# Kernel tuning notes

Measured on AMD Instinct MI355X. Metric: run time of the kernel, lower is better.

The kernel has to match this reference:

```python
import jax, jax.numpy as jnp
import numpy as np

EPS = 1e-5
NUM_HEADS = 12
HEAD_DIM = 64


def _split_heads(x, H, hd):
    B, S, _ = x.shape
    return x.reshape(B, S, H, hd).transpose(0, 2, 1, 3)  # [B,H,S,hd]


def _rope_rotate(x, pos, freqs):
    # x: [B,H,S,hd]; pos: [B,S,nd] int; freqs: [nd,H,hd//2]
    ang = jnp.einsum('bsd,dhf->bhsf', pos.astype(x.dtype), freqs)  # [B,H,S,hd//2]
    cos, sin = jnp.cos(ang), jnp.sin(ang)
    B, H, S, hd = x.shape
    xp = x.reshape(B, H, S, hd // 2, 2)
    xr, xi = xp[..., 0], xp[..., 1]
    out = jnp.stack([xr * cos - xi * sin, xr * sin + xi * cos], axis=-1)
    return out.reshape(B, H, S, hd)


def setup_inputs() -> dict:
    key = jax.random.key(0)
    ks = jax.random.split(key, 8)
    B, Sq, Sk, D = 4, 1024, 1024, 768
    return {
        'q': jax.random.normal(ks[0], (B, Sq, D), jnp.float32),
        'kv': jax.random.normal(ks[1], (B, Sk, D), jnp.float32),
        'posq': jax.random.randint(ks[2], (B, Sq, 2), 0, 32, jnp.int32),
        'posk': jax.random.randint(ks[3], (B, Sk, 2), 0, 32, jnp.int32),
        'w_norm': jnp.ones((D,), jnp.float32),
        'w_q': jax.random.normal(ks[4], (D, D), jnp.float32) * 0.02,
        'b_q': jnp.zeros((D,), jnp.float32),
        'w_kv': jax.random.normal(ks[5], (2 * D, D), jnp.float32) * 0.02,
        'b_kv': jnp.zeros((2 * D,), jnp.float32),
        'w_out': jax.random.normal(ks[6], (D, D), jnp.float32) * 0.02,
        'b_out': jnp.zeros((D,), jnp.float32),
        'freqs': jax.random.normal(ks[7], (2, NUM_HEADS, HEAD_DIM // 2), jnp.float32),
    }


def reference(q, kv, posq, posk, w_norm, w_q, b_q, w_kv, b_kv, w_out, b_out, freqs):
    B, Sq, D = q.shape
    H, hd = NUM_HEADS, HEAD_DIM
    # RMSNorm on q
    qn = q * jax.lax.rsqrt(jnp.mean(q * q, axis=-1, keepdims=True) + EPS) * w_norm
    # projections (torch F.linear: x @ W.T + b)
    qp = qn @ w_q.T + b_q
    kvp = kv @ w_kv.T + b_kv
    k, v = jnp.split(kvp, 2, axis=-1)
    qh = _split_heads(qp, H, hd)
    kh = _split_heads(k, H, hd)
    vh = _split_heads(v, H, hd)
    # ND mixed RoPE
    qh = _rope_rotate(qh, posq, freqs)
    kh = _rope_rotate(kh, posk, freqs)
    # SDPA
    scale = 1.0 / np.sqrt(hd)
    scores = jnp.einsum('bhqd,bhkd->bhqk', qh, kh) * scale
    attn = jax.nn.softmax(scores, axis=-1)
    o = jnp.einsum('bhqk,bhkd->bhqd', attn, vh)
    o = o.transpose(0, 2, 1, 3).reshape(B, Sq, H * hd)
    return o @ w_out.T + b_out
```

## Files before the change

kernel.cpp:

```cpp
#include <hip/hip_runtime.h>

#define B_   4
#define S_   1024
#define D_   768
#define H_   12
#define HD_  64
#define NROW (B_*S_)
#define RSTRIDE (H_*HD_)
#define NBH  (B_*H_)
#define LOG2E 1.44269504f

typedef __bf16 bf16_t;
typedef bf16_t bf16x8 __attribute__((ext_vector_type(8)));
typedef float  f32x4  __attribute__((ext_vector_type(4)));
typedef float  f32x16 __attribute__((ext_vector_type(16)));
typedef unsigned int u32x4 __attribute__((ext_vector_type(4)));

__device__ __forceinline__ unsigned short bf16b(float f){
  bf16_t b = (bf16_t)f;
  return __builtin_bit_cast(unsigned short, b);
}

__device__ __forceinline__ void gload16(const void* g, void* l){
  __builtin_amdgcn_global_load_lds(
      (const __attribute__((address_space(1))) void*)g,
      (__attribute__((address_space(3))) void*)l, 16, 0, 0);
}

__device__ __forceinline__ unsigned int cvtpk(float lo, float hi){
  unsigned int r;
  asm("v_cvt_pk_bf16_f32 %0, %1, %2" : "=v"(r) : "v"(lo), "v"(hi));
  return r;
}

__device__ __forceinline__ void plswap(unsigned int &a, unsigned int &b){
  asm volatile("v_permlane32_swap_b32 %0, %1" : "+v"(a), "+v"(b));
}

__global__ void prep_kernel(const float* __restrict__ q, const float* __restrict__ w_norm,
                            bf16_t* __restrict__ qn,
                            const float* __restrict__ wq,  bf16_t* __restrict__ wqb,
                            const float* __restrict__ wkv, bf16_t* __restrict__ wkvb,
                            const float* __restrict__ wo,  bf16_t* __restrict__ wob,
                            const float* __restrict__ kv,  bf16_t* __restrict__ kvb){
  int bid = blockIdx.x;
  if (bid < NROW){
    int row = bid;
    const float* src = q + (size_t)row*D_;
    float vals[3]; float ss = 0.f;
#pragma unroll
    for (int i=0;i<3;i++){ float v = src[threadIdx.x + i*256]; vals[i]=v; ss += v*v; }
#pragma unroll
    for (int m=1;m<64;m<<=1) ss += __shfl_xor(ss, m, 64);
    __shared__ float red[4];
    if ((threadIdx.x & 63) == 0) red[threadIdx.x>>6] = ss;
    __syncthreads();
    float tot = red[0]+red[1]+red[2]+red[3];
    float rs = rsqrtf(tot*(1.0f/D_) + 1e-5f);
#pragma unroll
    for (int i=0;i<3;i++){
      int c = threadIdx.x + i*256;
      qn[(size_t)row*D_ + c] = (bf16_t)(vals[i]*rs*w_norm[c]);
    }
  } else {
    int i = (bid - NROW)*256 + threadIdx.x;
    const int n0 = D_*D_/4, n1 = 2*D_*D_/4, n2 = D_*D_/4, n3 = NROW*D_/4;
    const float* s; bf16_t* d; int off;
    if (i < n0){ s = wq; d = wqb; off = i; }
    else if (i < n0+n1){ s = wkv; d = wkvb; off = i - n0; }
    else if (i < n0+n1+n2){ s = wo; d = wob; off = i - n0 - n1; }
    else if (i < n0+n1+n2+n3){ s = kv; d = kvb; off = i - n0 - n1 - n2; }
    else return;
    float4 v = reinterpret_cast<const float4*>(s)[off];
    ushort4 o;
    o.x = bf16b(v.x); o.y = bf16b(v.y); o.z = bf16b(v.z); o.w = bf16b(v.w);
    reinterpret_cast<ushort4*>(d)[off] = o;
  }
}

template<int TM, int TN>
__device__ __forceinline__ void stage_t(const bf16_t* __restrict__ A, const bf16_t* __restrict__ W,
                                        int K, int row0, int col0, int kt,
                                        bf16_t* As, bf16_t* Bs){
  const int tid = threadIdx.x;
  const int wv  = tid >> 6;
#pragma unroll
  for (int i=0;i<TM/32;i++){
    int c = i*256 + tid;
    int r = c >> 3, kc = (c & 7) ^ (r & 7);
    gload16(A + (size_t)(row0+r)*K + kt + kc*8, As + (size_t)(i*256 + wv*64)*8);
  }
#pragma unroll
  for (int i=0;i<TN/32;i++){
    int c = i*256 + tid;
    int r = c >> 3, kc = (c & 7) ^ (r & 7);
    gload16(W + (size_t)(col0+r)*K + kt + kc*8, Bs + (size_t)(i*256 + wv*64)*8);
  }
}

template<int TM, int TN>
__device__ __forceinline__ void compute_t(const bf16_t* As, const bf16_t* Bs,
                                          f32x4 (&acc)[TM/32][TN/32]){
  const int lane = threadIdx.x & 63;
  const int wv   = threadIdx.x >> 6;
  const int wr = wv >> 1, wc = wv & 1;
  const int l4 = lane >> 4, lm = lane & 15;
#pragma unroll
  for (int kk=0; kk<2; kk++){
    bf16x8 af[TM/32], bfr[TN/32];
#pragma unroll
    for (int mi=0;mi<TM/32;mi++){
      int r = wr*(TM/2) + mi*16 + lm;
      int s = (kk*4 + l4) ^ (r & 7);
      af[mi] = *reinterpret_cast<const bf16x8*>(As + r*64 + s*8);
    }
#pragma unroll
    for (int ni=0;ni<TN/32;ni++){
      int r = wc*(TN/2) + ni*16 + lm;
      int s = (kk*4 + l4) ^ (r & 7);
      bfr[ni] = *reinterpret_cast<const bf16x8*>(Bs + r*64 + s*8);
    }
#pragma unroll
    for (int mi=0;mi<TM/32;mi++)
#pragma unroll
      for (int ni=0;ni<TN/32;ni++)
        acc[mi][ni] = __builtin_amdgcn_mfma_f32_16x16x32_bf16(af[mi], bfr[ni], acc[mi][ni], 0,0,0);
  }
}

template<int TM, int TN>
__device__ __forceinline__ void gemm_core_db(const bf16_t* __restrict__ A, const bf16_t* __restrict__ W,
                                             int K, int row0, int col0,
                                             bf16_t* As0, bf16_t* As1, bf16_t* Bs0, bf16_t* Bs1,
                                             f32x4 (&acc)[TM/32][TN/32]){
  stage_t<TM,TN>(A, W, K, row0, col0, 0, As0, Bs0);
  __syncthreads();
  const int nt = K/64;
  bf16_t *Ac = As0, *An = As1, *Bc = Bs0, *Bn = Bs1;
  for (int t=0; t<nt; ++t){
    if (t+1 < nt)
      stage_t<TM,TN>(A, W, K, row0, col0, (t+1)*64, An, Bn);
    compute_t<TM,TN>(Ac, Bc, acc);
    __syncthreads();
    bf16_t* tmp;
    tmp = Ac; Ac = An; An = tmp;
    tmp = Bc; Bc = Bn; Bn = tmp;
  }
}

__global__ void gemm_kernel(const bf16_t* __restrict__ A, const bf16_t* __restrict__ W,
                            const float* __restrict__ bias, float* __restrict__ C,
                            int N, int K){
  __shared__ bf16_t As[2][64*64];
  __shared__ bf16_t Bs[2][64*64];
  int l = ((int)blockIdx.x & 7)*96 + ((int)blockIdx.x >> 3);
  int x = l & 63, y = l >> 6;
  f32x4 acc[2][2] = {};
  gemm_core_db<64,64>(A, W, K, x*64, y*64, As[0], As[1], Bs[0], Bs[1], acc);
  const int lane = threadIdx.x & 63;
  const int wv   = threadIdx.x >> 6;
  const int wr = wv >> 1, wc = wv & 1;
  const int l4 = lane >> 4, lm = lane & 15;
  const int row0 = x*64, col0 = y*64;
#pragma unroll
  for (int mi=0;mi<2;mi++){
#pragma unroll
    for (int ni=0;ni<2;ni++){
      int col = col0 + wc*32 + ni*16 + lm;
      float bv = bias[col];
#pragma unroll
      for (int j=0;j<4;j++){
        int row = row0 + wr*32 + mi*16 + l4*4 + j;
        C[(size_t)row*N + col] = acc[mi][ni][j] + bv;
      }
    }
  }
}

__device__ __forceinline__ void epi_rope(f32x4 (&acc)[2][4], const float* __restrict__ bias,
                                         const int* __restrict__ pos, const float* __restrict__ freqs,
                                         bf16_t* __restrict__ dst, int row0, int col0, float scale){
  const int lane = threadIdx.x & 63;
  const int wv   = threadIdx.x >> 6;
  const int wr = wv >> 1, wc = wv & 1;
  const int l4 = lane >> 4, lm = lane & 15;
  const int par = lm & 1;
#pragma unroll
  for (int ni=0;ni<4;ni++){
    int col = col0 + wc*64 + ni*16 + lm;
    int h = col >> 6, hd = col & 63, f = hd >> 1;
    float F1 = freqs[h*32 + f];
    float F2 = freqs[H_*32 + h*32 + f];
    float bv = bias[col];
    int cc = f >> 3, hi = (f >> 2) & 1;
    int ebase = cc*512 + hi*256 + (f&3)*2 + par;
#pragma unroll
    for (int mi=0;mi<2;mi++){
#pragma unroll
      for (int j=0;j<4;j++){
        int row = row0 + wr*32 + mi*16 + l4*4 + j;
        float v = acc[mi][ni][j] + bv;
        float vp = __shfl_xor(v, 1, 64);
        float p0 = (float)pos[row*2+0], p1 = (float)pos[row*2+1];
        float ang = p0*F1 + p1*F2;
        float sn, cs;
        __sincosf(ang, &sn, &cs);
        float out = (par ? (vp*sn + v*cs) : (v*cs - vp*sn)) * scale;
        int b = row >> 10, s = row & 1023;
        int bh = b*H_ + h, tile = s >> 5, lq = s & 31;
        dst[((size_t)(bh*32 + tile))*2048 + ebase + lq*8] = (bf16_t)out;
      }
    }
  }
}

__device__ __forceinline__ void epi_vpack(f32x4 (&acc)[2][4], const float* __restrict__ bias,
                                          bf16_t* __restrict__ vfrag, int row0, int col0){
  const int lane = threadIdx.x & 63;
  const int wv   = threadIdx.x >> 6;
  const int wr = wv >> 1, wc = wv & 1;
  const int l4 = lane >> 4, lm = lane & 15;
#pragma unroll
  for (int ni=0;ni<4;ni++){
    int col = col0 + wc*64 + ni*16 + lm;
    int vcol = col - D_;
    int h = vcol >> 6, d = vcol & 63;
    int dt = d >> 5, lq2 = d & 31;
    float bv = bias[col];
    int ebase = dt*1024 + lq2*8;
#pragma unroll
    for (int mi=0;mi<2;mi++){
#pragma unroll
      for (int j=0;j<4;j++){
        int row = row0 + wr*32 + mi*16 + l4*4 + j;
        int b = row >> 10, s = row & 1023;
        int bh = b*H_ + h;
        int kb = s >> 5, ks = (s >> 4) & 1, hi2 = (s >> 3) & 1, jj = s & 7;
        vfrag[((size_t)(bh*32 + kb))*2048 + ebase + ks*512 + hi2*256 + jj]
            = (bf16_t)(acc[mi][ni][j] + bv);
      }
    }
  }
}

__global__ void gemm_qkv_kernel(const bf16_t* __restrict__ qn, const bf16_t* __restrict__ kvb,
                                const bf16_t* __restrict__ wq, const bf16_t* __restrict__ wkv,
                                const float* __restrict__ bq, const float* __restrict__ bkv,
                                const int* __restrict__ posq, const int* __restrict__ posk,
                                const float* __restrict__ freqs,
                                bf16_t* __restrict__ qh, bf16_t* __restrict__ kh,
                                bf16_t* __restrict__ vfrag){
  __shared__ bf16_t As[2][64*64];
  __shared__ bf16_t Bs[2][128*64];
  int l = ((int)blockIdx.x & 7)*144 + ((int)blockIdx.x >> 3);
  int x = l & 63, y = l >> 6;
  f32x4 acc[2][4] = {};
  if (y < 6){
    gemm_core_db<64,128>(qn, wq, D_, x*64, y*128, As[0], As[1], Bs[0], Bs[1], acc);
    epi_rope(acc, bq, posq, freqs, qh, x*64, y*128, 0.125f*LOG2E);
  } else {
    int c0 = (y-6)*128;
    gemm_core_db<64,128>(kvb, wkv, D_, x*64, c0, As[0], As[1], Bs[0], Bs[1], acc);
    if (y < 12)
      epi_rope(acc, bkv, posk, freqs, kh, x*64, c0, 1.0f);
    else
      epi_vpack(acc, bkv, vfrag, x*64, c0);
  }
}

__device__ __forceinline__ void attn_step(const bf16x8 (&kf)[4], const bf16x8 (&vf)[4],
                                          const bf16x8 (&qf)[4], f32x16 (&acc_o)[2],
                                          float &psum){
  f32x16 accs = {};
#pragma unroll
  for (int c=0;c<4;c++)
    accs = __builtin_amdgcn_mfma_f32_32x32x16_bf16(kf[c], qf[c], accs, 0,0,0);
#pragma unroll
  for (int r=0;r<16;r++){
    float v = exp2f(accs[r]);
    accs[r] = v;
    psum += v;
  }
  bf16x8 pa[2];
#pragma unroll
  for (int ks=0;ks<2;ks++){
    const int base = ks*8;
    unsigned int a0 = cvtpk(accs[base+0], accs[base+1]);
    unsigned int a1 = cvtpk(accs[base+2], accs[base+3]);
    unsigned int b0 = cvtpk(accs[base+4], accs[base+5]);
    unsigned int b1 = cvtpk(accs[base+6], accs[base+7]);
    plswap(a0, b0);
    plswap(a1, b1);
    u32x4 w; w[0]=a0; w[1]=a1; w[2]=b0; w[3]=b1;
    pa[ks] = __builtin_bit_cast(bf16x8, w);
  }
#pragma unroll
  for (int dt=0;dt<2;dt++)
#pragma unroll
    for (int ks=0;ks<2;ks++)
      acc_o[dt] = __builtin_amdgcn_mfma_f32_32x32x16_bf16(pa[ks], vf[dt*2+ks], acc_o[dt], 0,0,0);
}

__global__ __launch_bounds__(256, 3)
void attn_kernel(const bf16_t* __restrict__ Qf, const bf16_t* __restrict__ Kf,
                 const bf16_t* __restrict__ Vf, bf16_t* __restrict__ Oh){
  const int lane = threadIdx.x & 63;
  const int wv   = threadIdx.x >> 6;
  const int hi = lane >> 5, lq = lane & 31;
  int l = ((int)blockIdx.x & 7)*192 + ((int)blockIdx.x >> 3);
  const int bh = l >> 5;
  const int qt = l & 31;
  const int q0 = qt*32;
  const int b = bh / H_, h = bh % H_;
  const size_t headoff = ((size_t)b*S_*H_ + h)*HD_;

  __shared__ float part[4][64][33];
  __shared__ float ps[4][32];

  bf16x8 qf[4];
  {
    const bf16_t* qp_ = Qf + (size_t)(bh*32 + qt)*2048 + lane*8;
#pragma unroll
    for (int c=0;c<4;c++)
      qf[c] = *reinterpret_cast<const bf16x8*>(qp_ + c*512);
  }

  const bf16_t* kbase = Kf + ((size_t)bh*32 + wv*8)*2048 + lane*8;
  const bf16_t* vbase = Vf + ((size_t)bh*32 + wv*8)*2048 + lane*8;

  float psum = 0.f;
  f32x16 acc_o[2] = {};

  bf16x8 kfA[4], kfB[4], vf[4];
#pragma unroll
  for (int c=0;c<4;c++)
    kfA[c] = *reinterpret_cast<const bf16x8*>(kbase + c*512);

#pragma unroll
  for (int t=0; t<4; ++t){
    {
      const bf16_t* vp = vbase + (size_t)(2*t)*2048;
#pragma unroll
      for (int j=0;j<4;j++) vf[j] = *reinterpret_cast<const bf16x8*>(vp + j*512);
      const bf16_t* kp = kbase + (size_t)(2*t+1)*2048;
#pragma unroll
      for (int c=0;c<4;c++) kfB[c] = *reinterpret_cast<const bf16x8*>(kp + c*512);
      attn_step(kfA, vf, qf, acc_o, psum);
    }
    {
      const bf16_t* vp = vbase + (size_t)(2*t+1)*2048;
#pragma unroll
      for (int j=0;j<4;j++) vf[j] = *reinterpret_cast<const bf16x8*>(vp + j*512);
      if (t < 3){
        const bf16_t* kp = kbase + (size_t)(2*t+2)*2048;
#pragma unroll
        for (int c=0;c<4;c++) kfA[c] = *reinterpret_cast<const bf16x8*>(kp + c*512);
      }
      attn_step(kfB, vf, qf, acc_o, psum);
    }
  }

  float tp = psum + __shfl_xor(psum, 32, 64);
#pragma unroll
  for (int dt=0;dt<2;dt++)
#pragma unroll
    for (int r=0;r<16;r++)
      part[wv][lane][dt*16+r] = acc_o[dt][r];
  if (lane < 32) ps[wv][lq] = tp;
  __syncthreads();

  const int dt = wv >> 1;
  const int rbase = (wv & 1)*8;
  float tot = ps[0][lq] + ps[1][lq] + ps[2][lq] + ps[3][lq];
  float inv = 1.0f / tot;

  bf16_t* obase = Oh + headoff;
#pragma unroll
  for (int ri=0;ri<8;ri++){
    int r = rbase + ri;
    float s = part[0][lane][dt*16+r] + part[1][lane][dt*16+r]
            + part[2][lane][dt*16+r] + part[3][lane][dt*16+r];
    float invr = __shfl(inv, (r&3) + 8*(r>>2) + 4*hi, 64);
    int qq = q0 + (r&3) + 8*(r>>2) + 4*hi;
    obase[(size_t)qq*RSTRIDE + dt*32 + lq] = (bf16_t)(s*invr);
  }
}

extern "C" void kernel_launch(void* const* d_in, const int* in_sizes, int n_in,
                              void* d_out, int out_size, void* d_ws, size_t ws_size,
                              hipStream_t stream) {
  const float* q      = (const float*)d_in[0];
  const float* kv     = (const float*)d_in[1];
  const int*   posq   = (const int*)d_in[2];
  const int*   posk   = (const int*)d_in[3];
  const float* w_norm = (const float*)d_in[4];
  const float* w_q    = (const float*)d_in[5];
  const float* b_q    = (const float*)d_in[6];
  const float* w_kv   = (const float*)d_in[7];
  const float* b_kv   = (const float*)d_in[8];
  const float* w_out  = (const float*)d_in[9];
  const float* b_out  = (const float*)d_in[10];
  const float* freqs  = (const float*)d_in[11];
  float* out = (float*)d_out;

  char* p = (char*)d_ws;
  bf16_t* qn   = (bf16_t*)p; p += (size_t)NROW*D_*2;
  bf16_t* kvb  = (bf16_t*)p; p += (size_t)NROW*D_*2;
  bf16_t* wqb  = (bf16_t*)p; p += (size_t)D_*D_*2;
  bf16_t* wkvb = (bf16_t*)p; p += (size_t)2*D_*D_*2;
  bf16_t* wob  = (bf16_t*)p; p += (size_t)D_*D_*2;
  bf16_t* qh   = (bf16_t*)p; p += (size_t)NROW*D_*2;
  bf16_t* kh   = (bf16_t*)p; p += (size_t)NROW*D_*2;
  bf16_t* vt   = (bf16_t*)p; p += (size_t)NBH*HD_*S_*2;
  bf16_t* oh   = (bf16_t*)p; p += (size_t)NROW*D_*2;

  prep_kernel<<<NROW + 5376, 256, 0, stream>>>(q, w_norm, qn,
                                               w_q, wqb, w_kv, wkvb, w_out, wob, kv, kvb);
  gemm_qkv_kernel<<<1152, 256, 0, stream>>>(qn, kvb, wqb, wkvb, b_q, b_kv,
                                            posq, posk, freqs, qh, kh, vt);
  attn_kernel<<<1536, 256, 0, stream>>>(qh, kh, vt, oh);
  gemm_kernel<<<768, 256, 0, stream>>>(oh, wob, b_out, out, D_, D_);
}
```

Before: 74.90 us.

## Pre-pack QKV GEMM operands into MFMA fragment layout and drop LDS staging

The prep kernel now writes the normalized q, kv and the q/kv weights in a 32-row by 16-k fragment layout that matches the 32x32x16 MFMA operand order. The QKV GEMM kernel then loads fragments directly from global memory into registers, with no LDS double buffering, uses 128x128 block tiles with 32x32 MFMAs, and fuses RoPE and V packing with paired stores. This removes LDS traffic and barriers from the projection GEMM. The trade-off is scattered stores in prep and reliance on L2 for operand reuse across blocks.

```diff
diff --git a/kernel.cpp b/kernel.cpp
--- a/kernel.cpp
+++ b/kernel.cpp
@@ -37,12 +37,16 @@
   asm volatile("v_permlane32_swap_b32 %0, %1" : "+v"(a), "+v"(b));
 }
 
+__device__ __forceinline__ size_t frag48_addr(int row, int k){
+  return ((size_t)((row>>5)*48 + (k>>4)))*512 + ((k>>3)&1)*256 + (row&31)*8 + (k&7);
+}
+
 __global__ void prep_kernel(const float* __restrict__ q, const float* __restrict__ w_norm,
-                            bf16_t* __restrict__ qn,
-                            const float* __restrict__ wq,  bf16_t* __restrict__ wqb,
-                            const float* __restrict__ wkv, bf16_t* __restrict__ wkvb,
+                            bf16_t* __restrict__ qnf,
+                            const float* __restrict__ wq,  bf16_t* __restrict__ wqf,
+                            const float* __restrict__ wkv, bf16_t* __restrict__ wkvf,
                             const float* __restrict__ wo,  bf16_t* __restrict__ wob,
-                            const float* __restrict__ kv,  bf16_t* __restrict__ kvb){
+                            const float* __restrict__ kv,  bf16_t* __restrict__ kvbf){
   int bid = blockIdx.x;
   if (bid < NROW){
     int row = bid;
@@ -60,21 +64,130 @@
 #pragma unroll
     for (int i=0;i<3;i++){
       int c = threadIdx.x + i*256;
-      qn[(size_t)row*D_ + c] = (bf16_t)(vals[i]*rs*w_norm[c]);
+      qnf[frag48_addr(row, c)] = (bf16_t)(vals[i]*rs*w_norm[c]);
     }
   } else {
     int i = (bid - NROW)*256 + threadIdx.x;
     const int n0 = D_*D_/4, n1 = 2*D_*D_/4, n2 = D_*D_/4, n3 = NROW*D_/4;
-    const float* s; bf16_t* d; int off;
-    if (i < n0){ s = wq; d = wqb; off = i; }
-    else if (i < n0+n1){ s = wkv; d = wkvb; off = i - n0; }
-    else if (i < n0+n1+n2){ s = wo; d = wob; off = i - n0 - n1; }
-    else if (i < n0+n1+n2+n3){ s = kv; d = kvb; off = i - n0 - n1 - n2; }
-    else return;
-    float4 v = reinterpret_cast<const float4*>(s)[off];
-    ushort4 o;
-    o.x = bf16b(v.x); o.y = bf16b(v.y); o.z = bf16b(v.z); o.w = bf16b(v.w);
-    reinterpret_cast<ushort4*>(d)[off] = o;
+    if (i < n0 + n1 + n3 && i < n0 + n1 || i >= n0 + n1 + n2 || i < n0){}
+    if (i < n0){
+      float4 v = reinterpret_cast<const float4*>(wq)[i];
+      int e0 = i*4, row = e0/768, k = e0%768;
+      ushort4 o; o.x=bf16b(v.x); o.y=bf16b(v.y); o.z=bf16b(v.z); o.w=bf16b(v.w);
+      *reinterpret_cast<ushort4*>(wqf + frag48_addr(row,k)) = o;
+    } else if (i < n0+n1){
+      int off = i - n0;
+      float4 v = reinterpret_cast<const float4*>(wkv)[off];
+      int e0 = off*4, row = e0/768, k = e0%768;
+      ushort4 o; o.x=bf16b(v.x); o.y=bf16b(v.y); o.z=bf16b(v.z); o.w=bf16b(v.w);
+      *reinterpret_cast<ushort4*>(wkvf + frag48_addr(row,k)) = o;
+    } else if (i < n0+n1+n2){
+      int off = i - n0 - n1;
+      float4 v = reinterpret_cast<const float4*>(wo)[off];
+      ushort4 o; o.x=bf16b(v.x); o.y=bf16b(v.y); o.z=bf16b(v.z); o.w=bf16b(v.w);
+      reinterpret_cast<ushort4*>(wob)[off] = o;
+    } else if (i < n0+n1+n2+n3){
+      int off = i - n0 - n1 - n2;
+      float4 v = reinterpret_cast<const float4*>(kv)[off];
+      int e0 = off*4, row = e0/768, k = e0%768;
+      ushort4 o; o.x=bf16b(v.x); o.y=bf16b(v.y); o.z=bf16b(v.z); o.w=bf16b(v.w);
+      *reinterpret_cast<ushort4*>(kvbf + frag48_addr(row,k)) = o;
+    }
+  }
+}
+
+__global__ __launch_bounds__(256, 3)
+void gemm_qkv_kernel(const bf16_t* __restrict__ qnf, const bf16_t* __restrict__ kvbf,
+                     const bf16_t* __restrict__ wqf, const bf16_t* __restrict__ wkvf,
+                     const float* __restrict__ bq, const float* __restrict__ bkv,
+                     const int* __restrict__ posq, const int* __restrict__ posk,
+                     const float* __restrict__ freqs,
+                     bf16_t* __restrict__ qh, bf16_t* __restrict__ kh,
+                     bf16_t* __restrict__ vfrag){
+  const int lane = threadIdx.x & 63;
+  const int wv   = threadIdx.x >> 6;
+  const int hi = lane >> 5, lq = lane & 31;
+  int l = ((int)blockIdx.x & 7)*72 + ((int)blockIdx.x >> 3);
+  const int x = l & 31, y = l >> 5;
+  const int wr = wv >> 1, wc = wv & 1;
+  const int rt0 = x*4 + wr*2;
+  const bf16_t* Af; const bf16_t* Wf; const float* bias; const int* pos; int ntbase;
+  if (y < 6){ Af = qnf; Wf = wqf;  bias = bq;  pos = posq; ntbase = y*4 + wc*2; }
+  else      { Af = kvbf; Wf = wkvf; bias = bkv; pos = posk; ntbase = (y-6)*4 + wc*2; }
+
+  const bf16_t* a0 = Af + ((size_t)(rt0  )*48)*512 + lane*8;
+  const bf16_t* a1 = Af + ((size_t)(rt0+1)*48)*512 + lane*8;
+  const bf16_t* w0 = Wf + ((size_t)(ntbase  )*48)*512 + lane*8;
+  const bf16_t* w1 = Wf + ((size_t)(ntbase+1)*48)*512 + lane*8;
+
+  f32x16 acc[2][2] = {};
+#pragma unroll 4
+  for (int c=0;c<48;c++){
+    bf16x8 A0 = *reinterpret_cast<const bf16x8*>(a0 + (size_t)c*512);
+    bf16x8 A1 = *reinterpret_cast<const bf16x8*>(a1 + (size_t)c*512);
+    bf16x8 W0 = *reinterpret_cast<const bf16x8*>(w0 + (size_t)c*512);
+    bf16x8 W1 = *reinterpret_cast<const bf16x8*>(w1 + (size_t)c*512);
+    acc[0][0] = __builtin_amdgcn_mfma_f32_32x32x16_bf16(W0, A0, acc[0][0], 0,0,0);
+    acc[0][1] = __builtin_amdgcn_mfma_f32_32x32x16_bf16(W0, A1, acc[0][1], 0,0,0);
+    acc[1][0] = __builtin_amdgcn_mfma_f32_32x32x16_bf16(W1, A0, acc[1][0], 0,0,0);
+    acc[1][1] = __builtin_amdgcn_mfma_f32_32x32x16_bf16(W1, A1, acc[1][1], 0,0,0);
+  }
+
+  if (y < 12){
+    const float scale = (y < 6) ? 0.125f*LOG2E : 1.0f;
+    bf16_t* dst = (y < 6) ? qh : kh;
+#pragma unroll
+    for (int rt=0;rt<2;rt++){
+      int row = (rt0+rt)*32 + lq;
+      float p0 = (float)pos[row*2+0], p1 = (float)pos[row*2+1];
+      int bb = row >> 10;
+      int tile = (row & 1023) >> 5;
+#pragma unroll
+      for (int nt=0;nt<2;nt++){
+        int ntg = ntbase + nt;
+#pragma unroll
+        for (int rp=0;rp<8;rp++){
+          int r = rp*2;
+          int n = ntg*32 + (r&3) + 8*(r>>2) + 4*hi;
+          int h = n >> 6, d = n & 63, f = d >> 1;
+          float F1 = freqs[h*32 + f];
+          float F2 = freqs[H_*32 + h*32 + f];
+          float ang = p0*F1 + p1*F2;
+          float sn, cs;
+          __sincosf(ang, &sn, &cs);
+          float ve = acc[nt][rt][r]   + bias[n];
+          float vo = acc[nt][rt][r+1] + bias[n+1];
+          float oe = (ve*cs - vo*sn)*scale;
+          float oo = (ve*sn + vo*cs)*scale;
+          int cc = d >> 4, hi2 = (d >> 3) & 1, jj = d & 7;
+          size_t base = ((size_t)((bb*H_ + h)*32 + tile))*2048 + cc*512 + hi2*256 + lq*8 + jj;
+          ushort2 o; o.x = bf16b(oe); o.y = bf16b(oo);
+          *reinterpret_cast<ushort2*>(dst + base) = o;
+        }
+      }
+    }
+  } else {
+#pragma unroll
+    for (int rt=0;rt<2;rt++){
+      int s_ = (rt0+rt)*32 + lq;
+      int bb = s_ >> 10;
+      int kb = (s_ & 1023) >> 5;
+      int ks = (lq >> 4) & 1, hi2 = (lq >> 3) & 1, jj = lq & 7;
+#pragma unroll
+      for (int nt=0;nt<2;nt++){
+        int ntg = ntbase + nt;
+#pragma unroll
+        for (int r=0;r<16;r++){
+          int n = ntg*32 + (r&3) + 8*(r>>2) + 4*hi;
+          int nv = n - D_;
+          int h = nv >> 6, d = nv & 63;
+          float v = acc[nt][rt][r] + bias[n];
+          size_t addr = ((size_t)((bb*H_ + h)*32 + kb))*2048
+                      + (d>>5)*1024 + ks*512 + hi2*256 + (d&31)*8 + jj;
+          vfrag[addr] = (bf16_t)v;
+        }
+      }
+    }
   }
 }
 
@@ -125,26 +238,6 @@
 #pragma unroll
       for (int ni=0;ni<TN/32;ni++)
         acc[mi][ni] = __builtin_amdgcn_mfma_f32_16x16x32_bf16(af[mi], bfr[ni], acc[mi][ni], 0,0,0);
-  }
-}
-
-template<int TM, int TN>
-__device__ __forceinline__ void gemm_core_db(const bf16_t* __restrict__ A, const bf16_t* __restrict__ W,
-                                             int K, int row0, int col0,
-                                             bf16_t* As0, bf16_t* As1, bf16_t* Bs0, bf16_t* Bs1,
-                                             f32x4 (&acc)[TM/32][TN/32]){
-  stage_t<TM,TN>(A, W, K, row0, col0, 0, As0, Bs0);
-  __syncthreads();
-  const int nt = K/64;
-  bf16_t *Ac = As0, *An = As1, *Bc = Bs0, *Bn = Bs1;
-  for (int t=0; t<nt; ++t){
-    if (t+1 < nt)
-      stage_t<TM,TN>(A, W, K, row0, col0, (t+1)*64, An, Bn);
-    compute_t<TM,TN>(Ac, Bc, acc);
-    __syncthreads();
-    bf16_t* tmp;
-    tmp = Ac; Ac = An; An = tmp;
-    tmp = Bc; Bc = Bn; Bn = tmp;
   }
 }
 
@@ -156,7 +249,16 @@
   int l = ((int)blockIdx.x & 7)*96 + ((int)blockIdx.x >> 3);
   int x = l & 63, y = l >> 6;
   f32x4 acc[2][2] = {};
-  gemm_core_db<64,64>(A, W, K, x*64, y*64, As[0], As[1], Bs[0], Bs[1], acc);
+  stage_t<64,64>(A, W, K, x*64, y*64, 0, As[0], Bs[0]);
+  __syncthreads();
+  const int nt = K/64;
+  for (int t=0; t<nt; ++t){
+    int cur = t & 1;
+    if (t+1 < nt)
+      stage_t<64,64>(A, W, K, x*64, y*64, (t+1)*64, As[cur^1], Bs[cur^1]);
+    compute_t<64,64>(As[cur], Bs[cur], acc);
+    __syncthreads();
+  }
   const int lane = threadIdx.x & 63;
   const int wv   = threadIdx.x >> 6;
   const int wr = wv >> 1, wc = wv & 1;
@@ -174,97 +276,6 @@
         C[(size_t)row*N + col] = acc[mi][ni][j] + bv;
       }
     }
-  }
-}
-
-__device__ __forceinline__ void epi_rope(f32x4 (&acc)[2][4], const float* __restrict__ bias,
-                                         const int* __restrict__ pos, const float* __restrict__ freqs,
-                                         bf16_t* __restrict__ dst, int row0, int col0, float scale){
-  const int lane = threadIdx.x & 63;
-  const int wv   = threadIdx.x >> 6;
-  const int wr = wv >> 1, wc = wv & 1;
-  const int l4 = lane >> 4, lm = lane & 15;
-  const int par = lm & 1;
-#pragma unroll
-  for (int ni=0;ni<4;ni++){
-    int col = col0 + wc*64 + ni*16 + lm;
-    int h = col >> 6, hd = col & 63, f = hd >> 1;
-    float F1 = freqs[h*32 + f];
-    float F2 = freqs[H_*32 + h*32 + f];
-    float bv = bias[col];
-    int cc = f >> 3, hi = (f >> 2) & 1;
-    int ebase = cc*512 + hi*256 + (f&3)*2 + par;
-#pragma unroll
-    for (int mi=0;mi<2;mi++){
-#pragma unroll
-      for (int j=0;j<4;j++){
-        int row = row0 + wr*32 + mi*16 + l4*4 + j;
-        float v = acc[mi][ni][j] + bv;
-        float vp = __shfl_xor(v, 1, 64);
-        float p0 = (float)pos[row*2+0], p1 = (float)pos[row*2+1];
-        float ang = p0*F1 + p1*F2;
-        float sn, cs;
-        __sincosf(ang, &sn, &cs);
-        float out = (par ? (vp*sn + v*cs) : (v*cs - vp*sn)) * scale;
-        int b = row >> 10, s = row & 1023;
-        int bh = b*H_ + h, tile = s >> 5, lq = s & 31;
-        dst[((size_t)(bh*32 + tile))*2048 + ebase + lq*8] = (bf16_t)out;
-      }
-    }
-  }
-}
-
-__device__ __forceinline__ void epi_vpack(f32x4 (&acc)[2][4], const float* __restrict__ bias,
-                                          bf16_t* __restrict__ vfrag, int row0, int col0){
-  const int lane = threadIdx.x & 63;
-  const int wv   = threadIdx.x >> 6;
-  const int wr = wv >> 1, wc = wv & 1;
-  const int l4 = lane >> 4, lm = lane & 15;
-#pragma unroll
-  for (int ni=0;ni<4;ni++){
-    int col = col0 + wc*64 + ni*16 + lm;
-    int vcol = col - D_;
-    int h = vcol >> 6, d = vcol & 63;
-    int dt = d >> 5, lq2 = d & 31;
-    float bv = bias[col];
-    int ebase = dt*1024 + lq2*8;
-#pragma unroll
-    for (int mi=0;mi<2;mi++){
-#pragma unroll
-      for (int j=0;j<4;j++){
-        int row = row0 + wr*32 + mi*16 + l4*4 + j;
-        int b = row >> 10, s = row & 1023;
-        int bh = b*H_ + h;
-        int kb = s >> 5, ks = (s >> 4) & 1, hi2 = (s >> 3) & 1, jj = s & 7;
-        vfrag[((size_t)(bh*32 + kb))*2048 + ebase + ks*512 + hi2*256 + jj]
-            = (bf16_t)(acc[mi][ni][j] + bv);
-      }
-    }
-  }
-}
-
-__global__ void gemm_qkv_kernel(const bf16_t* __restrict__ qn, const bf16_t* __restrict__ kvb,
-                                const bf16_t* __restrict__ wq, const bf16_t* __restrict__ wkv,
-                                const float* __restrict__ bq, const float* __restrict__ bkv,
-                                const int* __restrict__ posq, const int* __restrict__ posk,
-                                const float* __restrict__ freqs,
-                                bf16_t* __restrict__ qh, bf16_t* __restrict__ kh,
-                                bf16_t* __restrict__ vfrag){
-  __shared__ bf16_t As[2][64*64];
-  __shared__ bf16_t Bs[2][128*64];
-  int l = ((int)blockIdx.x & 7)*144 + ((int)blockIdx.x >> 3);
-  int x = l & 63, y = l >> 6;
-  f32x4 acc[2][4] = {};
-  if (y < 6){
-    gemm_core_db<64,128>(qn, wq, D_, x*64, y*128, As[0], As[1], Bs[0], Bs[1], acc);
-    epi_rope(acc, bq, posq, freqs, qh, x*64, y*128, 0.125f*LOG2E);
-  } else {
-    int c0 = (y-6)*128;
-    gemm_core_db<64,128>(kvb, wkv, D_, x*64, c0, As[0], As[1], Bs[0], Bs[1], acc);
-    if (y < 12)
-      epi_rope(acc, bkv, posk, freqs, kh, x*64, c0, 1.0f);
-    else
-      epi_vpack(acc, bkv, vfrag, x*64, c0);
   }
 }
 
@@ -404,20 +415,20 @@
   float* out = (float*)d_out;
 
   char* p = (char*)d_ws;
-  bf16_t* qn   = (bf16_t*)p; p += (size_t)NROW*D_*2;
-  bf16_t* kvb  = (bf16_t*)p; p += (size_t)NROW*D_*2;
-  bf16_t* wqb  = (bf16_t*)p; p += (size_t)D_*D_*2;
-  bf16_t* wkvb = (bf16_t*)p; p += (size_t)2*D_*D_*2;
+  bf16_t* qnf  = (bf16_t*)p; p += (size_t)NROW*D_*2;
+  bf16_t* kvbf = (bf16_t*)p; p += (size_t)NROW*D_*2;
+  bf16_t* wqf  = (bf16_t*)p; p += (size_t)D_*D_*2;
+  bf16_t* wkvf = (bf16_t*)p; p += (size_t)2*D_*D_*2;
   bf16_t* wob  = (bf16_t*)p; p += (size_t)D_*D_*2;
   bf16_t* qh   = (bf16_t*)p; p += (size_t)NROW*D_*2;
   bf16_t* kh   = (bf16_t*)p; p += (size_t)NROW*D_*2;
   bf16_t* vt   = (bf16_t*)p; p += (size_t)NBH*HD_*S_*2;
   bf16_t* oh   = (bf16_t*)p; p += (size_t)NROW*D_*2;
 
-  prep_kernel<<<NROW + 5376, 256, 0, stream>>>(q, w_norm, qn,
-                                               w_q, wqb, w_kv, wkvb, w_out, wob, kv, kvb);
-  gemm_qkv_kernel<<<1152, 256, 0, stream>>>(qn, kvb, wqb, wkvb, b_q, b_kv,
-                                            posq, posk, freqs, qh, kh, vt);
+  prep_kernel<<<NROW + 5376, 256, 0, stream>>>(q, w_norm, qnf,
+                                               w_q, wqf, w_kv, wkvf, w_out, wob, kv, kvbf);
+  gemm_qkv_kernel<<<576, 256, 0, stream>>>(qnf, kvbf, wqf, wkvf, b_q, b_kv,
+                                           posq, posk, freqs, qh, kh, vt);
   attn_kernel<<<1536, 256, 0, stream>>>(qh, kh, vt, oh);
   gemm_kernel<<<768, 256, 0, stream>>>(oh, wob, b_out, out, D_, D_);
 }
```

Measured after the change: 89.86 us. +20.0%, slower.

## Use single-buffered 128-wide K tiles in QKV GEMM instead of double buffering

Applied to the files above, without the earlier changes.

The fused QKV projection GEMM now stages 128-wide K slices into one LDS buffer, with a sync before and after each compute, instead of double-buffered 64-wide slices. This halves the number of K iterations and barriers and unifies the operand selection before a single loop. The cost is that global-to-LDS loads no longer overlap MFMA compute, so memory latency is exposed on every tile. The generic gemm_kernel only has its double-buffer helper inlined, with index-based buffer selection.

```diff
diff --git a/kernel.cpp b/kernel.cpp
--- a/kernel.cpp
+++ b/kernel.cpp
@@ -79,6 +79,60 @@
 }
 
 template<int TM, int TN>
+__device__ __forceinline__ void stage128(const bf16_t* __restrict__ A, const bf16_t* __restrict__ W,
+                                         int K, int row0, int col0, int kt,
+                                         bf16_t* As, bf16_t* Bs){
+  const int tid = threadIdx.x;
+  const int wv  = tid >> 6;
+#pragma unroll
+  for (int i=0;i<TM/16;i++){
+    int c = i*256 + tid;
+    int r = c >> 4, sl = c & 15;
+    int kc = ((sl & 7) ^ (r & 7)) | (sl & 8);
+    gload16(A + (size_t)(row0+r)*K + kt + kc*8, As + (size_t)(i*256 + wv*64)*8);
+  }
+#pragma unroll
+  for (int i=0;i<TN/16;i++){
+    int c = i*256 + tid;
+    int r = c >> 4, sl = c & 15;
+    int kc = ((sl & 7) ^ (r & 7)) | (sl & 8);
+    gload16(W + (size_t)(col0+r)*K + kt + kc*8, Bs + (size_t)(i*256 + wv*64)*8);
+  }
+}
+
+template<int TM, int TN>
+__device__ __forceinline__ void compute128(const bf16_t* As, const bf16_t* Bs,
+                                           f32x4 (&acc)[TM/32][TN/32]){
+  const int lane = threadIdx.x & 63;
+  const int wv   = threadIdx.x >> 6;
+  const int wr = wv >> 1, wc = wv & 1;
+  const int l4 = lane >> 4, lm = lane & 15;
+#pragma unroll
+  for (int kk=0; kk<4; kk++){
+    bf16x8 af[TM/32], bfr[TN/32];
+#pragma unroll
+    for (int mi=0;mi<TM/32;mi++){
+      int r = wr*(TM/2) + mi*16 + lm;
+      int t = kk*4 + l4;
+      int s = ((t & 7) ^ (r & 7)) | (t & 8);
+      af[mi] = *reinterpret_cast<const bf16x8*>(As + r*128 + s*8);
+    }
+#pragma unroll
+    for (int ni=0;ni<TN/32;ni++){
+      int r = wc*(TN/2) + ni*16 + lm;
+      int t = kk*4 + l4;
+      int s = ((t & 7) ^ (r & 7)) | (t & 8);
+      bfr[ni] = *reinterpret_cast<const bf16x8*>(Bs + r*128 + s*8);
+    }
+#pragma unroll
+    for (int mi=0;mi<TM/32;mi++)
+#pragma unroll
+      for (int ni=0;ni<TN/32;ni++)
+        acc[mi][ni] = __builtin_amdgcn_mfma_f32_16x16x32_bf16(af[mi], bfr[ni], acc[mi][ni], 0,0,0);
+  }
+}
+
+template<int TM, int TN>
 __device__ __forceinline__ void stage_t(const bf16_t* __restrict__ A, const bf16_t* __restrict__ W,
                                         int K, int row0, int col0, int kt,
                                         bf16_t* As, bf16_t* Bs){
@@ -125,26 +179,6 @@
 #pragma unroll
       for (int ni=0;ni<TN/32;ni++)
         acc[mi][ni] = __builtin_amdgcn_mfma_f32_16x16x32_bf16(af[mi], bfr[ni], acc[mi][ni], 0,0,0);
-  }
-}
-
-template<int TM, int TN>
-__device__ __forceinline__ void gemm_core_db(const bf16_t* __restrict__ A, const bf16_t* __restrict__ W,
-                                             int K, int row0, int col0,
-                                             bf16_t* As0, bf16_t* As1, bf16_t* Bs0, bf16_t* Bs1,
-                                             f32x4 (&acc)[TM/32][TN/32]){
-  stage_t<TM,TN>(A, W, K, row0, col0, 0, As0, Bs0);
-  __syncthreads();
-  const int nt = K/64;
-  bf16_t *Ac = As0, *An = As1, *Bc = Bs0, *Bn = Bs1;
-  for (int t=0; t<nt; ++t){
-    if (t+1 < nt)
-      stage_t<TM,TN>(A, W, K, row0, col0, (t+1)*64, An, Bn);
-    compute_t<TM,TN>(Ac, Bc, acc);
-    __syncthreads();
-    bf16_t* tmp;
-    tmp = Ac; Ac = An; An = tmp;
-    tmp = Bc; Bc = Bn; Bn = tmp;
   }
 }
 
@@ -156,7 +190,16 @@
   int l = ((int)blockIdx.x & 7)*96 + ((int)blockIdx.x >> 3);
   int x = l & 63, y = l >> 6;
   f32x4 acc[2][2] = {};
-  gemm_core_db<64,64>(A, W, K, x*64, y*64, As[0], As[1], Bs[0], Bs[1], acc);
+  stage_t<64,64>(A, W, K, x*64, y*64, 0, As[0], Bs[0]);
+  __syncthreads();
+  const int nt = K/64;
+  for (int t=0; t<nt; ++t){
+    int cur = t & 1;
+    if (t+1 < nt)
+      stage_t<64,64>(A, W, K, x*64, y*64, (t+1)*64, As[cur^1], Bs[cur^1]);
+    compute_t<64,64>(As[cur], Bs[cur], acc);
+    __syncthreads();
+  }
   const int lane = threadIdx.x & 63;
   const int wv   = threadIdx.x >> 6;
   const int wr = wv >> 1, wc = wv & 1;
@@ -250,22 +293,28 @@
                                 const float* __restrict__ freqs,
                                 bf16_t* __restrict__ qh, bf16_t* __restrict__ kh,
                                 bf16_t* __restrict__ vfrag){
-  __shared__ bf16_t As[2][64*64];
-  __shared__ bf16_t Bs[2][128*64];
+  __shared__ bf16_t As[64*128];
+  __shared__ bf16_t Bs[128*128];
   int l = ((int)blockIdx.x & 7)*144 + ((int)blockIdx.x >> 3);
   int x = l & 63, y = l >> 6;
   f32x4 acc[2][4] = {};
-  if (y < 6){
-    gemm_core_db<64,128>(qn, wq, D_, x*64, y*128, As[0], As[1], Bs[0], Bs[1], acc);
-    epi_rope(acc, bq, posq, freqs, qh, x*64, y*128, 0.125f*LOG2E);
-  } else {
-    int c0 = (y-6)*128;
-    gemm_core_db<64,128>(kvb, wkv, D_, x*64, c0, As[0], As[1], Bs[0], Bs[1], acc);
-    if (y < 12)
-      epi_rope(acc, bkv, posk, freqs, kh, x*64, c0, 1.0f);
-    else
-      epi_vpack(acc, bkv, vfrag, x*64, c0);
-  }
+  const bf16_t* A; const bf16_t* W; int c0;
+  if (y < 6){ A = qn;  W = wq;  c0 = y*128; }
+  else      { A = kvb; W = wkv; c0 = (y-6)*128; }
+
+  for (int kt = 0; kt < D_; kt += 128){
+    stage128<64,128>(A, W, D_, x*64, c0, kt, As, Bs);
+    __syncthreads();
+    compute128<64,128>(As, Bs, acc);
+    __syncthreads();
+  }
+
+  if (y < 6)
+    epi_rope(acc, bq, posq, freqs, qh, x*64, c0, 0.125f*LOG2E);
+  else if (y < 12)
+    epi_rope(acc, bkv, posk, freqs, kh, x*64, c0, 1.0f);
+  else
+    epi_vpack(acc, bkv, vfrag, x*64, c0);
 }
 
 __device__ __forceinline__ void attn_step(const bf16x8 (&kf)[4], const bf16x8 (&vf)[4],
```

Result: slower. 77.75 us (+3.8%).
